# Optimization experiments

Hardware: AMD Instinct MI355X
Metric: run time of the kernel (lower is better)

The kernel has to match this reference:

```python
import math
import jax, jax.numpy as jnp
import numpy as np

N_HEADS = 8
FACTOR = 1


def setup_inputs() -> dict:
    key = jax.random.key(0)
    ks = jax.random.split(key, 8)
    B, L, D = 8, 2048, 512
    scale = 0.05
    return {
        "queries": jax.random.normal(ks[0], (B, L, D), jnp.float32),
        "keys": jax.random.normal(ks[1], (B, L, D), jnp.float32),
        "values": jax.random.normal(ks[2], (B, L, D), jnp.float32),
        "Wq": jax.random.normal(ks[3], (D, D), jnp.float32) * scale,
        "bq": jnp.zeros((D,), jnp.float32),
        "Wk": jax.random.normal(ks[4], (D, D), jnp.float32) * scale,
        "bk": jnp.zeros((D,), jnp.float32),
        "Wv": jax.random.normal(ks[5], (D, D), jnp.float32) * scale,
        "bv": jnp.zeros((D,), jnp.float32),
        "Wo": jax.random.normal(ks[6], (D, D), jnp.float32) * scale,
        "bo": jnp.zeros((D,), jnp.float32),
    }


def _autocorrelation(q, k, v):
    # q,k,v: [B, L, H, E]; L == S assumed (as built in setup_inputs)
    B, L, H, E = q.shape
    qp = jnp.transpose(q, (0, 2, 3, 1))  # [B,H,E,L]
    kp = jnp.transpose(k, (0, 2, 3, 1))
    vp = jnp.transpose(v, (0, 2, 3, 1))
    q_fft = jnp.fft.rfft(qp, axis=-1)
    k_fft = jnp.fft.rfft(kp, axis=-1)
    corr = jnp.fft.irfft(q_fft * jnp.conj(k_fft), n=L, axis=-1)  # [B,H,E,L]

    # training-path time-delay aggregation
    top_k = int(FACTOR * math.log(L))  # static python int
    mean_value = corr.mean(axis=(1, 2))  # [B, L]
    _, index = jax.lax.top_k(mean_value.mean(axis=0), top_k)  # [K] global delays
    weights = mean_value[:, index]  # [B, K]
    tmp_corr = jax.nn.softmax(weights, axis=-1)  # [B, K]
    # roll(v, -d) along last axis == gather at (t + d) mod L
    idx = (jnp.arange(L)[None, :] + index[:, None]) % L  # [K, L]
    patterns = vp[..., idx]  # [B,H,E,K,L]
    delays_agg = jnp.einsum('bhekl,bk->bhel', patterns, tmp_corr)  # [B,H,E,L]
    return jnp.transpose(delays_agg, (0, 3, 1, 2))  # [B,L,H,E]


def reference(queries, keys, values, Wq, bq, Wk, bk, Wv, bv, Wo, bo):
    B, L, Dm = queries.shape
    H = N_HEADS
    q = (queries @ Wq + bq).reshape(B, L, H, -1)
    k = (keys @ Wk + bk).reshape(B, L, H, -1)
    v = (values @ Wv + bv).reshape(B, L, H, -1)
    out = _autocorrelation(q, k, v).reshape(B, L, -1)
    return out @ Wo + bo
```

## Files before the change

kernel.cpp:

```cpp
#include <hip/hip_runtime.h>
#include <stdint.h>

#define BATCH 8
#define L_SEQ 2048
#define D_MODEL 512
#define TOPK 7
#define BM 128
#define BN 128
#define BK 32
#define LK 40
#define LT 136

typedef _Float16 f16x8 __attribute__((ext_vector_type(8)));
typedef __attribute__((ext_vector_type(4))) float f32x4;
typedef unsigned short u16;
typedef unsigned int u32;

__device__ __forceinline__ u16 f2h(float f) {
    union { _Float16 h; u16 u; } v; v.h = (_Float16)f; return v.u;
}
__device__ __forceinline__ float h2f(u16 b) {
    union { u16 u; _Float16 h; } v; v.u = b; return (float)v.h;
}

__device__ __forceinline__ void load_lds16(const u16* g, u16* l) {
    __builtin_amdgcn_global_load_lds(
        (const __attribute__((address_space(1))) u32*)(g),
        (__attribute__((address_space(3))) u32*)(l), 16, 0, 0);
}

__global__ __launch_bounds__(256) void gemm_qkv(
    const float* __restrict__ Xq, const float* __restrict__ Xk, const float* __restrict__ Xv,
    const u16* __restrict__ Wqt, const u16* __restrict__ Wkt, const u16* __restrict__ Wvt,
    const float* __restrict__ bq, const float* __restrict__ bk, const float* __restrict__ bv,
    u16* __restrict__ QT, u16* __restrict__ KT, u16* __restrict__ Vout)
{
    __shared__ __align__(16) u16 lA[BM * LK];
    __shared__ __align__(16) u16 lB[BN * LK];
    __shared__ __align__(16) u16 lT[64 * LT];

    const int tid = threadIdx.x;
    const int bn = blockIdx.x, bm = blockIdx.y, z = blockIdx.z;
    const int lane = tid & 63, wave = tid >> 6;
    const int wm = wave >> 1, wn = wave & 1;
    const int l15 = lane & 15, quad = lane >> 4;

    const float* A  = (z == 0) ? Xq  : (z == 1) ? Xk  : Xv;
    const u16*   Bt = (z == 0) ? Wqt : (z == 1) ? Wkt : Wvt;
    const float* bias = (z == 0) ? bq : (z == 1) ? bk : bv;

    f32x4 acc[4][4] = {};
    const int K = D_MODEL, N = D_MODEL;

    for (int k0 = 0; k0 < K; k0 += BK) {
        #pragma unroll
        for (int j = 0; j < 4; ++j) {
            int idx = tid + j * 256;
            int row = idx >> 3, c4 = (idx & 7) * 4;
            float4 va = *(const float4*)(A + (long)(bm * BM + row) * K + k0 + c4);
            ushort4 pa;
            pa.x = f2h(va.x); pa.y = f2h(va.y); pa.z = f2h(va.z); pa.w = f2h(va.w);
            *(ushort4*)&lA[row * LK + c4] = pa;
        }
        #pragma unroll
        for (int j = 0; j < 2; ++j) {
            int idx = tid + j * 256;
            int row = idx >> 2, c8 = (idx & 3) * 8;
            *(uint4*)&lB[row * LK + c8] =
                *(const uint4*)(Bt + (long)(bn * BN + row) * K + k0 + c8);
        }
        __syncthreads();

        f16x8 fa[4], fb[4];
        #pragma unroll
        for (int i = 0; i < 4; ++i)
            fa[i] = *(const f16x8*)&lA[(wm * 64 + i * 16 + l15) * LK + quad * 8];
        #pragma unroll
        for (int j = 0; j < 4; ++j)
            fb[j] = *(const f16x8*)&lB[(wn * 64 + j * 16 + l15) * LK + quad * 8];
        #pragma unroll
        for (int i = 0; i < 4; ++i)
            #pragma unroll
            for (int j = 0; j < 4; ++j)
                acc[i][j] = __builtin_amdgcn_mfma_f32_16x16x32_f16(fa[i], fb[j], acc[i][j], 0, 0, 0);
        __syncthreads();
    }

    if (z < 2) {
        u16* out = (z == 0) ? QT : KT;
        const int t0 = (bm * BM) & (L_SEQ - 1);
        const int bb = (bm * BM) >> 11;
        #pragma unroll
        for (int h = 0; h < 2; ++h) {
            __syncthreads();
            if (wn == h) {
                #pragma unroll
                for (int j = 0; j < 4; ++j) {
                    int dloc = j * 16 + l15;
                    float bvv = bias[bn * BN + h * 64 + dloc];
                    #pragma unroll
                    for (int i = 0; i < 4; ++i) {
                        int trow = wm * 64 + i * 16 + quad * 4;
                        #pragma unroll
                        for (int r = 0; r < 4; ++r)
                            lT[dloc * LT + trow + r] = f2h(acc[i][j][r] + bvv);
                    }
                }
            }
            __syncthreads();
            int dloc = tid >> 2, q4 = tid & 3;
            long base = ((long)(bb * D_MODEL + bn * BN + h * 64 + dloc)) * L_SEQ + t0;
            #pragma unroll
            for (int s = 0; s < 4; ++s) {
                int c = q4 * 4 + s;
                *(uint4*)(out + base + c * 8) = *(const uint4*)&lT[dloc * LT + c * 8];
            }
        }
    } else {
        #pragma unroll
        for (int i = 0; i < 4; ++i) {
            int row = bm * BM + wm * 64 + i * 16 + quad * 4;
            #pragma unroll
            for (int j = 0; j < 4; ++j) {
                int col = bn * BN + wn * 64 + j * 16 + l15;
                float bvv = bias[col];
                #pragma unroll
                for (int r = 0; r < 4; ++r)
                    Vout[(long)(row + r) * N + col] = f2h(acc[i][j][r] + bvv);
            }
        }
    }
}

__global__ __launch_bounds__(256, 4) void gemm_f16_out32(
    const u16* __restrict__ A, const u16* __restrict__ Bt,
    const float* __restrict__ bias, float* __restrict__ Cp, int N, int K)
{
    __shared__ __align__(16) u16 lA[BM * BK];
    __shared__ __align__(16) u16 lB[BN * BK];

    const int tid = threadIdx.x;
    const int bn = blockIdx.x, bm = blockIdx.y;
    const int lane = tid & 63, wave = tid >> 6;
    const int wm = wave >> 1, wn = wave & 1;
    const int l15 = lane & 15, quad = lane >> 4;

    const int s0 = wave * 64 + lane, s1 = s0 + 256;
    const int r0 = s0 >> 2, c0 = (s0 & 3) ^ ((r0 >> 1) & 3);
    const int r1 = s1 >> 2, c1 = (s1 & 3) ^ ((r1 >> 1) & 3);
    const u16* gA0 = A + (long)(bm * BM + r0) * K + c0 * 8;
    const u16* gA1 = A + (long)(bm * BM + r1) * K + c1 * 8;
    const u16* gB0 = Bt + (long)(bn * BN + r0) * K + c0 * 8;
    const u16* gB1 = Bt + (long)(bn * BN + r1) * K + c1 * 8;
    u16* lA0 = &lA[wave * 512]; u16* lA1 = &lA[2048 + wave * 512];
    u16* lB0 = &lB[wave * 512]; u16* lB1 = &lB[2048 + wave * 512];

    f32x4 acc[4][4] = {};

    for (int k0 = 0; k0 < K; k0 += BK) {
        load_lds16(gA0, lA0); load_lds16(gA1, lA1);
        load_lds16(gB0, lB0); load_lds16(gB1, lB1);
        gA0 += BK; gA1 += BK; gB0 += BK; gB1 += BK;
        __syncthreads();

        f16x8 fa[4], fb[4];
        #pragma unroll
        for (int i = 0; i < 4; ++i) {
            int m = wm * 64 + i * 16 + l15;
            int cs = quad ^ ((m >> 1) & 3);
            fa[i] = *(const f16x8*)&lA[m * 32 + cs * 8];
        }
        #pragma unroll
        for (int j = 0; j < 4; ++j) {
            int n = wn * 64 + j * 16 + l15;
            int cs = quad ^ ((n >> 1) & 3);
            fb[j] = *(const f16x8*)&lB[n * 32 + cs * 8];
        }
        #pragma unroll
        for (int i = 0; i < 4; ++i)
            #pragma unroll
            for (int j = 0; j < 4; ++j)
                acc[i][j] = __builtin_amdgcn_mfma_f32_16x16x32_f16(fa[i], fb[j], acc[i][j], 0, 0, 0);
        __syncthreads();
    }

    #pragma unroll
    for (int i = 0; i < 4; ++i) {
        int row = bm * BM + wm * 64 + i * 16 + quad * 4;
        #pragma unroll
        for (int j = 0; j < 4; ++j) {
            int col = bn * BN + wn * 64 + j * 16 + l15;
            float bvv = bias[col];
            #pragma unroll
            for (int r = 0; r < 4; ++r)
                Cp[(long)(row + r) * N + col] = acc[i][j][r] + bvv;
        }
    }
}

__global__ __launch_bounds__(256) void fft_corr_fwd(
    const u16* __restrict__ QT, const u16* __restrict__ KT, float* __restrict__ S)
{
    __shared__ float Zr[2048], Zi[2048];
    __shared__ float Sr[2048], Si[2048];
    __shared__ float Twr[1024], Twi[1024];
    const int tid = threadIdx.x;
    const int b = blockIdx.x >> 6, dg = blockIdx.x & 63;

    #pragma unroll
    for (int j = 0; j < 4; ++j) {
        int i = tid + j * 256;
        float ang = -6.28318530717958647692f * (float)i * (1.0f / 2048.0f);
        float sn, cs; __sincosf(ang, &sn, &cs);
        Twr[i] = cs; Twi[i] = sn;
    }
    #pragma unroll
    for (int j = 0; j < 8; ++j) { Sr[tid + j * 256] = 0.f; Si[tid + j * 256] = 0.f; }

    for (int g = 0; g < 8; ++g) {
        int d = dg * 8 + g;
        const u16* qrow = QT + ((long)b * D_MODEL + d) * L_SEQ;
        const u16* krow = KT + ((long)b * D_MODEL + d) * L_SEQ;
        __syncthreads();
        union { uint4 u; _Float16 h[8]; } xq, xk;
        xq.u = *(const uint4*)(qrow + tid * 8);
        xk.u = *(const uint4*)(krow + tid * 8);
        #pragma unroll
        for (int j = 0; j < 8; ++j) {
            int t = tid * 8 + j;
            int tr = (int)(__brev((unsigned)t) >> 21);
            Zr[tr] = (float)xq.h[j];
            Zi[tr] = (float)xk.h[j];
        }
        __syncthreads();
        for (int s = 0; s < 11; ++s) {
            #pragma unroll
            for (int j = 0; j < 4; ++j) {
                int idx = tid + j * 256;
                int pos = idx & ((1 << s) - 1);
                int i0 = ((idx >> s) << (s + 1)) + pos;
                int i1 = i0 + (1 << s);
                float wr = Twr[pos << (10 - s)], wi = Twi[pos << (10 - s)];
                float ar = Zr[i0], ai = Zi[i0];
                float br = Zr[i1], bi = Zi[i1];
                float tr_ = br * wr - bi * wi;
                float ti_ = br * wi + bi * wr;
                Zr[i0] = ar + tr_; Zi[i0] = ai + ti_;
                Zr[i1] = ar - tr_; Zi[i1] = ai - ti_;
            }
            __syncthreads();
        }
        #pragma unroll
        for (int j = 0; j < 8; ++j) {
            int f = tid + j * 256;
            int fm = (2048 - f) & 2047;
            float Xr = Zr[f], Xi = Zi[f], Xmr = Zr[fm], Xmi = Zi[fm];
            float qr = 0.5f * (Xr + Xmr), qi = 0.5f * (Xi - Xmi);
            float dr = Xr - Xmr,          di = Xi + Xmi;
            float kr = 0.5f * di,         ki = -0.5f * dr;
            Sr[f] += qr * kr + qi * ki;
            Si[f] += qi * kr - qr * ki;
        }
    }
    __syncthreads();
    #pragma unroll
    for (int j = 0; j < 8; ++j) {
        int f = tid + j * 256;
        atomicAdd(&S[((long)b * 2048 + f) * 2 + 0], Sr[f]);
        atomicAdd(&S[((long)b * 2048 + f) * 2 + 1], Si[f]);
    }
}

__global__ __launch_bounds__(256) void fft_corr_inv(
    const float* __restrict__ S, float* __restrict__ raw)
{
    __shared__ float Zr[2048], Zi[2048];
    __shared__ float Twr[1024], Twi[1024];
    const int tid = threadIdx.x;
    const int b = blockIdx.x;

    #pragma unroll
    for (int j = 0; j < 4; ++j) {
        int i = tid + j * 256;
        float ang = 6.28318530717958647692f * (float)i * (1.0f / 2048.0f);
        float sn, cs; __sincosf(ang, &sn, &cs);
        Twr[i] = cs; Twi[i] = sn;
    }
    #pragma unroll
    for (int j = 0; j < 8; ++j) {
        int f = tid + j * 256;
        int fr = (int)(__brev((unsigned)f) >> 21);
        Zr[fr] = S[((long)b * 2048 + f) * 2 + 0];
        Zi[fr] = S[((long)b * 2048 + f) * 2 + 1];
    }
    __syncthreads();
    for (int s = 0; s < 11; ++s) {
        #pragma unroll
        for (int j = 0; j < 4; ++j) {
            int idx = tid + j * 256;
            int pos = idx & ((1 << s) - 1);
            int i0 = ((idx >> s) << (s + 1)) + pos;
            int i1 = i0 + (1 << s);
            float wr = Twr[pos << (10 - s)], wi = Twi[pos << (10 - s)];
            float ar = Zr[i0], ai = Zi[i0];
            float br = Zr[i1], bi = Zi[i1];
            float tr_ = br * wr - bi * wi;
            float ti_ = br * wi + bi * wr;
            Zr[i0] = ar + tr_; Zi[i0] = ai + ti_;
            Zr[i1] = ar - tr_; Zi[i1] = ai - ti_;
        }
        __syncthreads();
    }
    #pragma unroll
    for (int j = 0; j < 8; ++j) {
        int t = tid + j * 256;
        raw[(long)b * 2048 + t] = Zr[t] * (1.0f / 2048.0f);
    }
}

__global__ __launch_bounds__(256) void transposeW(const float* __restrict__ src, u16* __restrict__ dst)
{
    __shared__ float t[32][33];
    int tx = threadIdx.x & 31, ty = threadIdx.x >> 5;
    int c0 = blockIdx.x * 32, r0 = blockIdx.y * 32;
    #pragma unroll
    for (int r = ty; r < 32; r += 8)
        t[r][tx] = src[(long)(r0 + r) * D_MODEL + c0 + tx];
    __syncthreads();
    #pragma unroll
    for (int r = ty; r < 32; r += 8)
        dst[(long)(c0 + r) * D_MODEL + r0 + tx] = f2h(t[tx][r]);
}

__global__ __launch_bounds__(256) void select_topk(
    const float* __restrict__ raw, int* __restrict__ selIdx, float* __restrict__ selW)
{
    __shared__ float g[L_SEQ];
    __shared__ float rv[256];
    __shared__ int   ri[256];
    __shared__ int   sidx[TOPK];
    __shared__ float wbuf[BATCH][TOPK];
    int tid = threadIdx.x;
    for (int t = tid; t < L_SEQ; t += 256) {
        float s = 0.0f;
        #pragma unroll
        for (int b = 0; b < BATCH; ++b) s += raw[b * L_SEQ + t];
        g[t] = s;
    }
    __syncthreads();
    for (int it = 0; it < TOPK; ++it) {
        float best = -1e30f; int bi = 0x7fffffff;
        for (int t = tid; t < L_SEQ; t += 256) {
            float v = g[t];
            if (v > best || (v == best && t < bi)) { best = v; bi = t; }
        }
        rv[tid] = best; ri[tid] = bi;
        __syncthreads();
        for (int s = 128; s > 0; s >>= 1) {
            if (tid < s) {
                float v2 = rv[tid + s]; int i2 = ri[tid + s];
                if (v2 > rv[tid] || (v2 == rv[tid] && i2 < ri[tid])) { rv[tid] = v2; ri[tid] = i2; }
            }
            __syncthreads();
        }
        if (tid == 0) { sidx[it] = ri[0]; g[ri[0]] = -1e30f; }
        __syncthreads();
    }
    if (tid < BATCH * TOPK) {
        int b = tid / TOPK, k = tid % TOPK;
        wbuf[b][k] = raw[b * L_SEQ + sidx[k]] * (1.0f / 512.0f);
    }
    __syncthreads();
    if (tid < BATCH) {
        float mx = -1e30f;
        #pragma unroll
        for (int k = 0; k < TOPK; ++k) mx = fmaxf(mx, wbuf[tid][k]);
        float e[TOPK]; float sum = 0.0f;
        #pragma unroll
        for (int k = 0; k < TOPK; ++k) { e[k] = expf(wbuf[tid][k] - mx); sum += e[k]; }
        #pragma unroll
        for (int k = 0; k < TOPK; ++k) selW[tid * TOPK + k] = e[k] / sum;
    }
    if (tid < TOPK) selIdx[tid] = sidx[tid];
}

__global__ __launch_bounds__(256) void gather_agg(
    const u16* __restrict__ V, const int* __restrict__ selIdx,
    const float* __restrict__ selW, u16* __restrict__ outB)
{
    __shared__ int si[TOPK];
    __shared__ float sw[TOPK];
    long flat = (long)blockIdx.x * 256 + threadIdx.x;
    int b  = (int)(flat >> 17);
    int l  = (int)((flat >> 6) & (L_SEQ - 1));
    int d8 = (int)(flat & 63);
    if (threadIdx.x < TOPK) {
        si[threadIdx.x] = selIdx[threadIdx.x];
        sw[threadIdx.x] = selW[b * TOPK + threadIdx.x];
    }
    __syncthreads();
    const uint4* v8 = (const uint4*)(V + (long)b * L_SEQ * D_MODEL);
    float a[8] = {0,0,0,0,0,0,0,0};
    #pragma unroll
    for (int k = 0; k < TOPK; ++k) {
        int src = (l + si[k]) & (L_SEQ - 1);
        union { uint4 u; _Float16 h[8]; } x;
        x.u = v8[src * 64 + d8];
        float w = sw[k];
        #pragma unroll
        for (int q = 0; q < 8; ++q) a[q] += w * (float)x.h[q];
    }
    union { uint4 u; _Float16 h[8]; } o;
    #pragma unroll
    for (int q = 0; q < 8; ++q) o.h[q] = (_Float16)a[q];
    ((uint4*)outB)[flat] = o.u;
}

extern "C" void kernel_launch(void* const* d_in, const int* in_sizes, int n_in,
                              void* d_out, int out_size, void* d_ws, size_t ws_size,
                              hipStream_t stream)
{
    (void)in_sizes; (void)n_in; (void)out_size; (void)ws_size;
    const float* Xq = (const float*)d_in[0];
    const float* Xk = (const float*)d_in[1];
    const float* Xv = (const float*)d_in[2];
    const float* Wq = (const float*)d_in[3];
    const float* bq = (const float*)d_in[4];
    const float* Wk = (const float*)d_in[5];
    const float* bk = (const float*)d_in[6];
    const float* Wv = (const float*)d_in[7];
    const float* bv = (const float*)d_in[8];
    const float* Wo = (const float*)d_in[9];
    const float* bo = (const float*)d_in[10];

    char* ws = (char*)d_ws;
    const long SLABH = (long)BATCH * L_SEQ * D_MODEL * sizeof(u16);
    u16* QT   = (u16*)(ws);
    u16* KT   = (u16*)(ws + SLABH);
    u16* Vf   = (u16*)(ws + 2 * SLABH);
    u16* attn = (u16*)(ws + 3 * SLABH);
    const long WSZ = (long)D_MODEL * D_MODEL;
    u16* Wt   = (u16*)(ws + 4 * SLABH);
    u16* Wqt = Wt + 0 * WSZ; u16* Wkt = Wt + 1 * WSZ;
    u16* Wvt = Wt + 2 * WSZ; u16* Wot = Wt + 3 * WSZ;
    float* S   = (float*)(ws + 4 * SLABH + 4 * WSZ * sizeof(u16));
    float* raw = S + (long)BATCH * L_SEQ * 2;
    int*   sIdx = (int*)(raw + (long)BATCH * L_SEQ);
    float* sW   = (float*)(sIdx + 8);

    dim3 tb(256);
    transposeW<<<dim3(16, 16), tb, 0, stream>>>(Wq, Wqt);
    transposeW<<<dim3(16, 16), tb, 0, stream>>>(Wk, Wkt);
    transposeW<<<dim3(16, 16), tb, 0, stream>>>(Wv, Wvt);
    transposeW<<<dim3(16, 16), tb, 0, stream>>>(Wo, Wot);
    hipMemsetAsync(S, 0, (long)BATCH * L_SEQ * 2 * sizeof(float), stream);

    dim3 gP(D_MODEL / BN, (BATCH * L_SEQ) / BM, 3);
    gemm_qkv<<<gP, tb, 0, stream>>>(Xq, Xk, Xv, Wqt, Wkt, Wvt, bq, bk, bv, QT, KT, Vf);

    fft_corr_fwd<<<dim3(512), tb, 0, stream>>>(QT, KT, S);
    fft_corr_inv<<<dim3(BATCH), tb, 0, stream>>>(S, raw);

    select_topk<<<1, tb, 0, stream>>>(raw, sIdx, sW);

    gather_agg<<<(BATCH * L_SEQ * D_MODEL / 8) / 256, tb, 0, stream>>>(Vf, sIdx, sW, attn);

    dim3 gO(D_MODEL / BN, (BATCH * L_SEQ) / BM, 1);
    gemm_f16_out32<<<gO, tb, 0, stream>>>(attn, Wot, bo, (float*)d_out, D_MODEL, D_MODEL);
}
```

Baseline: 357.9 us.

## Prefetch QKV GEMM tiles, radix-4 FFT, fuse inverse FFT with top-k, merge transposes

The QKV GEMM now loads the next K-tile into registers while the current tile is computed, aliases its LDS buffers, and remaps blocks to a 1D grid grouped for L2 locality. The FFT switches from radix-2 to radix-4 stages, halving the barrier count. The per-batch inverse FFT and the top-k kernel are merged into one finalize kernel. It runs a single inverse FFT on the batch-summed spectrum and computes the per-batch weights at the selected delays by direct DFT sums. The four weight-transpose launches become one. This cuts launches and synchronisations, but the finalize kernel is a single block doing serial DFT work.

```diff
diff --git a/kernel.cpp b/kernel.cpp
--- a/kernel.cpp
+++ b/kernel.cpp
@@ -19,9 +19,6 @@
 __device__ __forceinline__ u16 f2h(float f) {
     union { _Float16 h; u16 u; } v; v.h = (_Float16)f; return v.u;
 }
-__device__ __forceinline__ float h2f(u16 b) {
-    union { u16 u; _Float16 h; } v; v.u = b; return (float)v.h;
-}
 
 __device__ __forceinline__ void load_lds16(const u16* g, u16* l) {
     __builtin_amdgcn_global_load_lds(
@@ -35,12 +32,18 @@
     const float* __restrict__ bq, const float* __restrict__ bk, const float* __restrict__ bv,
     u16* __restrict__ QT, u16* __restrict__ KT, u16* __restrict__ Vout)
 {
-    __shared__ __align__(16) u16 lA[BM * LK];
-    __shared__ __align__(16) u16 lB[BN * LK];
-    __shared__ __align__(16) u16 lT[64 * LT];
+    __shared__ __align__(16) char smem[20480];
+    u16* lA = (u16*)smem;
+    u16* lB = (u16*)(smem + 10240);
+    u16* lT = (u16*)smem;
 
     const int tid = threadIdx.x;
-    const int bn = blockIdx.x, bm = blockIdx.y, z = blockIdx.z;
+    const int id = blockIdx.x;
+    const int bmL = id & 7;
+    const int bn  = (id >> 3) & 3;
+    const int bmH = (id >> 5) & 15;
+    const int z   = id >> 9;
+    const int bm  = bmH * 8 + bmL;
     const int lane = tid & 63, wave = tid >> 6;
     const int wm = wave >> 1, wn = wave & 1;
     const int l15 = lane & 15, quad = lane >> 4;
@@ -49,27 +52,48 @@
     const u16*   Bt = (z == 0) ? Wqt : (z == 1) ? Wkt : Wvt;
     const float* bias = (z == 0) ? bq : (z == 1) ? bk : bv;
 
+    float4 pA[4]; uint4 pB[2];
+    #pragma unroll
+    for (int j = 0; j < 4; ++j) {
+        int idx = tid + j * 256; int row = idx >> 3, c4 = (idx & 7) * 4;
+        pA[j] = *(const float4*)(A + (long)(bm * BM + row) * D_MODEL + c4);
+    }
+    #pragma unroll
+    for (int j = 0; j < 2; ++j) {
+        int idx = tid + j * 256; int row = idx >> 2, c8 = (idx & 3) * 8;
+        pB[j] = *(const uint4*)(Bt + (long)(bn * BN + row) * D_MODEL + c8);
+    }
+
     f32x4 acc[4][4] = {};
-    const int K = D_MODEL, N = D_MODEL;
-
-    for (int k0 = 0; k0 < K; k0 += BK) {
+
+    for (int k0 = 0; k0 < D_MODEL; k0 += BK) {
         #pragma unroll
         for (int j = 0; j < 4; ++j) {
-            int idx = tid + j * 256;
-            int row = idx >> 3, c4 = (idx & 7) * 4;
-            float4 va = *(const float4*)(A + (long)(bm * BM + row) * K + k0 + c4);
+            int idx = tid + j * 256; int row = idx >> 3, c4 = (idx & 7) * 4;
             ushort4 pa;
-            pa.x = f2h(va.x); pa.y = f2h(va.y); pa.z = f2h(va.z); pa.w = f2h(va.w);
+            pa.x = f2h(pA[j].x); pa.y = f2h(pA[j].y);
+            pa.z = f2h(pA[j].z); pa.w = f2h(pA[j].w);
             *(ushort4*)&lA[row * LK + c4] = pa;
         }
         #pragma unroll
         for (int j = 0; j < 2; ++j) {
-            int idx = tid + j * 256;
-            int row = idx >> 2, c8 = (idx & 3) * 8;
-            *(uint4*)&lB[row * LK + c8] =
-                *(const uint4*)(Bt + (long)(bn * BN + row) * K + k0 + c8);
-        }
-        __syncthreads();
+            int idx = tid + j * 256; int row = idx >> 2, c8 = (idx & 3) * 8;
+            *(uint4*)&lB[row * LK + c8] = pB[j];
+        }
+        __syncthreads();
+
+        if (k0 + BK < D_MODEL) {
+            #pragma unroll
+            for (int j = 0; j < 4; ++j) {
+                int idx = tid + j * 256; int row = idx >> 3, c4 = (idx & 7) * 4;
+                pA[j] = *(const float4*)(A + (long)(bm * BM + row) * D_MODEL + k0 + BK + c4);
+            }
+            #pragma unroll
+            for (int j = 0; j < 2; ++j) {
+                int idx = tid + j * 256; int row = idx >> 2, c8 = (idx & 3) * 8;
+                pB[j] = *(const uint4*)(Bt + (long)(bn * BN + row) * D_MODEL + k0 + BK + c8);
+            }
+        }
 
         f16x8 fa[4], fb[4];
         #pragma unroll
@@ -126,7 +150,7 @@
                 float bvv = bias[col];
                 #pragma unroll
                 for (int r = 0; r < 4; ++r)
-                    Vout[(long)(row + r) * N + col] = f2h(acc[i][j][r] + bvv);
+                    Vout[(long)(row + r) * D_MODEL + col] = f2h(acc[i][j][r] + bvv);
             }
         }
     }
@@ -198,6 +222,51 @@
     }
 }
 
+__device__ __forceinline__ void fft2048_lds(
+    float* Zr, float* Zi, const float* Twr, const float* Twi, int tid)
+{
+    #pragma unroll
+    for (int s = 0; s < 10; s += 2) {
+        #pragma unroll
+        for (int u = 0; u < 2; ++u) {
+            int idx = tid + u * 256;
+            int d1 = 1 << s;
+            int pos = idx & (d1 - 1);
+            int i0 = ((idx >> s) << (s + 2)) + pos;
+            float w1r = Twr[pos << (10 - s)], w1i = Twi[pos << (10 - s)];
+            float w2r = Twr[pos << (9 - s)],  w2i = Twi[pos << (9 - s)];
+            int p2 = pos + d1;
+            float w3r = Twr[p2 << (9 - s)],   w3i = Twi[p2 << (9 - s)];
+            float ar = Zr[i0],          ai = Zi[i0];
+            float br = Zr[i0 + d1],     bi = Zi[i0 + d1];
+            float cr = Zr[i0 + 2 * d1], ci = Zi[i0 + 2 * d1];
+            float dr = Zr[i0 + 3 * d1], di = Zi[i0 + 3 * d1];
+            float t1r = br * w1r - bi * w1i, t1i = br * w1i + bi * w1r;
+            float Ar = ar + t1r, Ai = ai + t1i, Br = ar - t1r, Bi = ai - t1i;
+            float t2r = dr * w1r - di * w1i, t2i = dr * w1i + di * w1r;
+            float Cr = cr + t2r, Ci = ci + t2i, Dr = cr - t2r, Di = ci - t2i;
+            float u1r = Cr * w2r - Ci * w2i, u1i = Cr * w2i + Ci * w2r;
+            float u2r = Dr * w3r - Di * w3i, u2i = Dr * w3i + Di * w3r;
+            Zr[i0]          = Ar + u1r; Zi[i0]          = Ai + u1i;
+            Zr[i0 + 2 * d1] = Ar - u1r; Zi[i0 + 2 * d1] = Ai - u1i;
+            Zr[i0 + d1]     = Br + u2r; Zi[i0 + d1]     = Bi + u2i;
+            Zr[i0 + 3 * d1] = Br - u2r; Zi[i0 + 3 * d1] = Bi - u2i;
+        }
+        __syncthreads();
+    }
+    #pragma unroll
+    for (int j = 0; j < 4; ++j) {
+        int idx = tid + j * 256;
+        float wr = Twr[idx], wi = Twi[idx];
+        float ar = Zr[idx], ai = Zi[idx];
+        float br = Zr[idx + 1024], bi = Zi[idx + 1024];
+        float tr = br * wr - bi * wi, ti = br * wi + bi * wr;
+        Zr[idx] = ar + tr; Zi[idx] = ai + ti;
+        Zr[idx + 1024] = ar - tr; Zi[idx + 1024] = ai - ti;
+    }
+    __syncthreads();
+}
+
 __global__ __launch_bounds__(256) void fft_corr_fwd(
     const u16* __restrict__ QT, const u16* __restrict__ KT, float* __restrict__ S)
 {
@@ -233,23 +302,7 @@
             Zi[tr] = (float)xk.h[j];
         }
         __syncthreads();
-        for (int s = 0; s < 11; ++s) {
-            #pragma unroll
-            for (int j = 0; j < 4; ++j) {
-                int idx = tid + j * 256;
-                int pos = idx & ((1 << s) - 1);
-                int i0 = ((idx >> s) << (s + 1)) + pos;
-                int i1 = i0 + (1 << s);
-                float wr = Twr[pos << (10 - s)], wi = Twi[pos << (10 - s)];
-                float ar = Zr[i0], ai = Zi[i0];
-                float br = Zr[i1], bi = Zi[i1];
-                float tr_ = br * wr - bi * wi;
-                float ti_ = br * wi + bi * wr;
-                Zr[i0] = ar + tr_; Zi[i0] = ai + ti_;
-                Zr[i1] = ar - tr_; Zi[i1] = ai - ti_;
-            }
-            __syncthreads();
-        }
+        fft2048_lds(Zr, Zi, Twr, Twi, tid);
         #pragma unroll
         for (int j = 0; j < 8; ++j) {
             int f = tid + j * 256;
@@ -271,13 +324,17 @@
     }
 }
 
-__global__ __launch_bounds__(256) void fft_corr_inv(
-    const float* __restrict__ S, float* __restrict__ raw)
+__global__ __launch_bounds__(256) void finalize(
+    const float* __restrict__ S, int* __restrict__ selIdx, float* __restrict__ selW)
 {
     __shared__ float Zr[2048], Zi[2048];
     __shared__ float Twr[1024], Twi[1024];
+    __shared__ float rv[256];
+    __shared__ int   ri[256];
+    __shared__ int   sidx[TOPK];
+    __shared__ float pbuf[256];
+    __shared__ float wbuf[BATCH][TOPK];
     const int tid = threadIdx.x;
-    const int b = blockIdx.x;
 
     #pragma unroll
     for (int j = 0; j < 4; ++j) {
@@ -289,69 +346,21 @@
     #pragma unroll
     for (int j = 0; j < 8; ++j) {
         int f = tid + j * 256;
+        float sr = 0.f, si = 0.f;
+        #pragma unroll
+        for (int b = 0; b < BATCH; ++b) {
+            sr += S[((long)b * 2048 + f) * 2 + 0];
+            si += S[((long)b * 2048 + f) * 2 + 1];
+        }
         int fr = (int)(__brev((unsigned)f) >> 21);
-        Zr[fr] = S[((long)b * 2048 + f) * 2 + 0];
-        Zi[fr] = S[((long)b * 2048 + f) * 2 + 1];
-    }
-    __syncthreads();
-    for (int s = 0; s < 11; ++s) {
-        #pragma unroll
-        for (int j = 0; j < 4; ++j) {
-            int idx = tid + j * 256;
-            int pos = idx & ((1 << s) - 1);
-            int i0 = ((idx >> s) << (s + 1)) + pos;
-            int i1 = i0 + (1 << s);
-            float wr = Twr[pos << (10 - s)], wi = Twi[pos << (10 - s)];
-            float ar = Zr[i0], ai = Zi[i0];
-            float br = Zr[i1], bi = Zi[i1];
-            float tr_ = br * wr - bi * wi;
-            float ti_ = br * wi + bi * wr;
-            Zr[i0] = ar + tr_; Zi[i0] = ai + ti_;
-            Zr[i1] = ar - tr_; Zi[i1] = ai - ti_;
-        }
-        __syncthreads();
-    }
-    #pragma unroll
-    for (int j = 0; j < 8; ++j) {
-        int t = tid + j * 256;
-        raw[(long)b * 2048 + t] = Zr[t] * (1.0f / 2048.0f);
-    }
-}
-
-__global__ __launch_bounds__(256) void transposeW(const float* __restrict__ src, u16* __restrict__ dst)
-{
-    __shared__ float t[32][33];
-    int tx = threadIdx.x & 31, ty = threadIdx.x >> 5;
-    int c0 = blockIdx.x * 32, r0 = blockIdx.y * 32;
-    #pragma unroll
-    for (int r = ty; r < 32; r += 8)
-        t[r][tx] = src[(long)(r0 + r) * D_MODEL + c0 + tx];
-    __syncthreads();
-    #pragma unroll
-    for (int r = ty; r < 32; r += 8)
-        dst[(long)(c0 + r) * D_MODEL + r0 + tx] = f2h(t[tx][r]);
-}
-
-__global__ __launch_bounds__(256) void select_topk(
-    const float* __restrict__ raw, int* __restrict__ selIdx, float* __restrict__ selW)
-{
-    __shared__ float g[L_SEQ];
-    __shared__ float rv[256];
-    __shared__ int   ri[256];
-    __shared__ int   sidx[TOPK];
-    __shared__ float wbuf[BATCH][TOPK];
-    int tid = threadIdx.x;
-    for (int t = tid; t < L_SEQ; t += 256) {
-        float s = 0.0f;
-        #pragma unroll
-        for (int b = 0; b < BATCH; ++b) s += raw[b * L_SEQ + t];
-        g[t] = s;
-    }
-    __syncthreads();
+        Zr[fr] = sr; Zi[fr] = si;
+    }
+    __syncthreads();
+    fft2048_lds(Zr, Zi, Twr, Twi, tid);
     for (int it = 0; it < TOPK; ++it) {
         float best = -1e30f; int bi = 0x7fffffff;
         for (int t = tid; t < L_SEQ; t += 256) {
-            float v = g[t];
+            float v = Zr[t];
             if (v > best || (v == best && t < bi)) { best = v; bi = t; }
         }
         rv[tid] = best; ri[tid] = bi;
@@ -363,25 +372,60 @@
             }
             __syncthreads();
         }
-        if (tid == 0) { sidx[it] = ri[0]; g[ri[0]] = -1e30f; }
-        __syncthreads();
-    }
+        if (tid == 0) { sidx[it] = ri[0]; Zr[ri[0]] = -1e30f; }
+        __syncthreads();
+    }
+    int pair = tid >> 2, i4 = tid & 3;
+    float part = 0.f;
+    if (pair < BATCH * TOPK) {
+        int b = pair / TOPK, k = pair % TOPK, tau = sidx[k];
+        for (int n = 0; n < 512; ++n) {
+            int f = i4 + 4 * n;
+            int m = (f * tau) & 2047;
+            float cr, ci;
+            if (m < 1024) { cr = Twr[m]; ci = Twi[m]; }
+            else          { cr = -Twr[m - 1024]; ci = -Twi[m - 1024]; }
+            part += S[((long)b * 2048 + f) * 2 + 0] * cr
+                  - S[((long)b * 2048 + f) * 2 + 1] * ci;
+        }
+    }
+    pbuf[tid] = part;
+    __syncthreads();
     if (tid < BATCH * TOPK) {
-        int b = tid / TOPK, k = tid % TOPK;
-        wbuf[b][k] = raw[b * L_SEQ + sidx[k]] * (1.0f / 512.0f);
+        float s = pbuf[tid * 4] + pbuf[tid * 4 + 1] + pbuf[tid * 4 + 2] + pbuf[tid * 4 + 3];
+        wbuf[tid / TOPK][tid % TOPK] = s * (1.0f / (2048.0f * 512.0f));
     }
     __syncthreads();
     if (tid < BATCH) {
         float mx = -1e30f;
         #pragma unroll
         for (int k = 0; k < TOPK; ++k) mx = fmaxf(mx, wbuf[tid][k]);
-        float e[TOPK]; float sum = 0.0f;
+        float e[TOPK]; float sum = 0.f;
         #pragma unroll
         for (int k = 0; k < TOPK; ++k) { e[k] = expf(wbuf[tid][k] - mx); sum += e[k]; }
         #pragma unroll
         for (int k = 0; k < TOPK; ++k) selW[tid * TOPK + k] = e[k] / sum;
     }
     if (tid < TOPK) selIdx[tid] = sidx[tid];
+}
+
+__global__ __launch_bounds__(256) void transposeW4(
+    const float* __restrict__ Wq, const float* __restrict__ Wk,
+    const float* __restrict__ Wv, const float* __restrict__ Wo, u16* __restrict__ dstBase)
+{
+    __shared__ float t[32][33];
+    const int z = blockIdx.z;
+    const float* src = (z == 0) ? Wq : (z == 1) ? Wk : (z == 2) ? Wv : Wo;
+    u16* dst = dstBase + (long)z * D_MODEL * D_MODEL;
+    int tx = threadIdx.x & 31, ty = threadIdx.x >> 5;
+    int c0 = blockIdx.x * 32, r0 = blockIdx.y * 32;
+    #pragma unroll
+    for (int r = ty; r < 32; r += 8)
+        t[r][tx] = src[(long)(r0 + r) * D_MODEL + c0 + tx];
+    __syncthreads();
+    #pragma unroll
+    for (int r = ty; r < 32; r += 8)
+        dst[(long)(c0 + r) * D_MODEL + r0 + tx] = f2h(t[tx][r]);
 }
 
 __global__ __launch_bounds__(256) void gather_agg(
@@ -444,24 +488,17 @@
     u16* Wqt = Wt + 0 * WSZ; u16* Wkt = Wt + 1 * WSZ;
     u16* Wvt = Wt + 2 * WSZ; u16* Wot = Wt + 3 * WSZ;
     float* S   = (float*)(ws + 4 * SLABH + 4 * WSZ * sizeof(u16));
-    float* raw = S + (long)BATCH * L_SEQ * 2;
-    int*   sIdx = (int*)(raw + (long)BATCH * L_SEQ);
+    int*   sIdx = (int*)(S + (long)BATCH * L_SEQ * 2);
     float* sW   = (float*)(sIdx + 8);
 
     dim3 tb(256);
-    transposeW<<<dim3(16, 16), tb, 0, stream>>>(Wq, Wqt);
-    transposeW<<<dim3(16, 16), tb, 0, stream>>>(Wk, Wkt);
-    transposeW<<<dim3(16, 16), tb, 0, stream>>>(Wv, Wvt);
-    transposeW<<<dim3(16, 16), tb, 0, stream>>>(Wo, Wot);
+    transposeW4<<<dim3(16, 16, 4), tb, 0, stream>>>(Wq, Wk, Wv, Wo, Wt);
     hipMemsetAsync(S, 0, (long)BATCH * L_SEQ * 2 * sizeof(float), stream);
 
-    dim3 gP(D_MODEL / BN, (BATCH * L_SEQ) / BM, 3);
-    gemm_qkv<<<gP, tb, 0, stream>>>(Xq, Xk, Xv, Wqt, Wkt, Wvt, bq, bk, bv, QT, KT, Vf);
+    gemm_qkv<<<dim3(1536), tb, 0, stream>>>(Xq, Xk, Xv, Wqt, Wkt, Wvt, bq, bk, bv, QT, KT, Vf);
 
     fft_corr_fwd<<<dim3(512), tb, 0, stream>>>(QT, KT, S);
-    fft_corr_inv<<<dim3(BATCH), tb, 0, stream>>>(S, raw);
-
-    select_topk<<<1, tb, 0, stream>>>(raw, sIdx, sW);
+    finalize<<<dim3(1), tb, 0, stream>>>(S, sIdx, sW);
 
     gather_agg<<<(BATCH * L_SEQ * D_MODEL / 8) / 256, tb, 0, stream>>>(Vf, sIdx, sW, attn);
 
```

After: 408.7 us. 14.2% more time.

## Fuse delay aggregation into output GEMM, radix-4 FFT stages, merge weight transposes

Applied to the files above, without the earlier changes.

Removes the separate gather_agg kernel and its attn intermediate by computing the weighted top-k delay sum directly while staging the A tile of the output projection GEMM. Replaces the radix-2 FFT loop with paired radix-4 stages to halve the number of LDS passes and barriers, and merges the four weight transposes into one launch. The fused GEMM recomputes the gather for each of the four N-tile blocks, which multiplies V reads, and it drops the async global_load_lds path for A.

```diff
diff --git a/kernel.cpp b/kernel.cpp
--- a/kernel.cpp
+++ b/kernel.cpp
@@ -19,9 +19,6 @@
 __device__ __forceinline__ u16 f2h(float f) {
     union { _Float16 h; u16 u; } v; v.h = (_Float16)f; return v.u;
 }
-__device__ __forceinline__ float h2f(u16 b) {
-    union { u16 u; _Float16 h; } v; v.u = b; return (float)v.h;
-}
 
 __device__ __forceinline__ void load_lds16(const u16* g, u16* l) {
     __builtin_amdgcn_global_load_lds(
@@ -50,14 +47,13 @@
     const float* bias = (z == 0) ? bq : (z == 1) ? bk : bv;
 
     f32x4 acc[4][4] = {};
-    const int K = D_MODEL, N = D_MODEL;
-
-    for (int k0 = 0; k0 < K; k0 += BK) {
+
+    for (int k0 = 0; k0 < D_MODEL; k0 += BK) {
         #pragma unroll
         for (int j = 0; j < 4; ++j) {
             int idx = tid + j * 256;
             int row = idx >> 3, c4 = (idx & 7) * 4;
-            float4 va = *(const float4*)(A + (long)(bm * BM + row) * K + k0 + c4);
+            float4 va = *(const float4*)(A + (long)(bm * BM + row) * D_MODEL + k0 + c4);
             ushort4 pa;
             pa.x = f2h(va.x); pa.y = f2h(va.y); pa.z = f2h(va.z); pa.w = f2h(va.w);
             *(ushort4*)&lA[row * LK + c4] = pa;
@@ -67,7 +63,7 @@
             int idx = tid + j * 256;
             int row = idx >> 2, c8 = (idx & 3) * 8;
             *(uint4*)&lB[row * LK + c8] =
-                *(const uint4*)(Bt + (long)(bn * BN + row) * K + k0 + c8);
+                *(const uint4*)(Bt + (long)(bn * BN + row) * D_MODEL + k0 + c8);
         }
         __syncthreads();
 
@@ -126,18 +122,21 @@
                 float bvv = bias[col];
                 #pragma unroll
                 for (int r = 0; r < 4; ++r)
-                    Vout[(long)(row + r) * N + col] = f2h(acc[i][j][r] + bvv);
+                    Vout[(long)(row + r) * D_MODEL + col] = f2h(acc[i][j][r] + bvv);
             }
         }
     }
 }
 
-__global__ __launch_bounds__(256, 4) void gemm_f16_out32(
-    const u16* __restrict__ A, const u16* __restrict__ Bt,
-    const float* __restrict__ bias, float* __restrict__ Cp, int N, int K)
-{
-    __shared__ __align__(16) u16 lA[BM * BK];
+__global__ __launch_bounds__(256) void gemm_out_fused(
+    const u16* __restrict__ V, const u16* __restrict__ Bt,
+    const int* __restrict__ selIdx, const float* __restrict__ selW,
+    const float* __restrict__ bias, float* __restrict__ Cp)
+{
+    __shared__ __align__(16) u16 lA[BM * LK];
     __shared__ __align__(16) u16 lB[BN * BK];
+    __shared__ int   si[TOPK];
+    __shared__ float sw[BATCH][TOPK];
 
     const int tid = threadIdx.x;
     const int bn = blockIdx.x, bm = blockIdx.y;
@@ -145,31 +144,50 @@
     const int wm = wave >> 1, wn = wave & 1;
     const int l15 = lane & 15, quad = lane >> 4;
 
+    if (tid < TOPK) si[tid] = selIdx[tid];
+    if (tid < BATCH * TOPK) sw[tid / TOPK][tid % TOPK] = selW[tid];
+
     const int s0 = wave * 64 + lane, s1 = s0 + 256;
     const int r0 = s0 >> 2, c0 = (s0 & 3) ^ ((r0 >> 1) & 3);
     const int r1 = s1 >> 2, c1 = (s1 & 3) ^ ((r1 >> 1) & 3);
-    const u16* gA0 = A + (long)(bm * BM + r0) * K + c0 * 8;
-    const u16* gA1 = A + (long)(bm * BM + r1) * K + c1 * 8;
-    const u16* gB0 = Bt + (long)(bn * BN + r0) * K + c0 * 8;
-    const u16* gB1 = Bt + (long)(bn * BN + r1) * K + c1 * 8;
-    u16* lA0 = &lA[wave * 512]; u16* lA1 = &lA[2048 + wave * 512];
+    const u16* gB0 = Bt + (long)(bn * BN + r0) * D_MODEL + c0 * 8;
+    const u16* gB1 = Bt + (long)(bn * BN + r1) * D_MODEL + c1 * 8;
     u16* lB0 = &lB[wave * 512]; u16* lB1 = &lB[2048 + wave * 512];
 
+    __syncthreads();
+
     f32x4 acc[4][4] = {};
 
-    for (int k0 = 0; k0 < K; k0 += BK) {
-        load_lds16(gA0, lA0); load_lds16(gA1, lA1);
+    for (int k0 = 0; k0 < D_MODEL; k0 += BK) {
         load_lds16(gB0, lB0); load_lds16(gB1, lB1);
-        gA0 += BK; gA1 += BK; gB0 += BK; gB1 += BK;
+        gB0 += BK; gB1 += BK;
+        #pragma unroll
+        for (int j = 0; j < 2; ++j) {
+            int idx = tid + j * 256;
+            int row = idx >> 2, c8 = (idx & 3) * 8;
+            int gr = bm * BM + row;
+            int b = gr >> 11, l = gr & (L_SEQ - 1);
+            float a[8] = {0,0,0,0,0,0,0,0};
+            #pragma unroll
+            for (int k = 0; k < TOPK; ++k) {
+                int src = (l + si[k]) & (L_SEQ - 1);
+                union { uint4 u; _Float16 h[8]; } x;
+                x.u = *(const uint4*)(V + ((long)b * L_SEQ + src) * D_MODEL + k0 + c8);
+                float w = sw[b][k];
+                #pragma unroll
+                for (int q = 0; q < 8; ++q) a[q] += w * (float)x.h[q];
+            }
+            union { uint4 u; u16 s[8]; } o;
+            #pragma unroll
+            for (int q = 0; q < 8; ++q) o.s[q] = f2h(a[q]);
+            *(uint4*)&lA[row * LK + c8] = o.u;
+        }
         __syncthreads();
 
         f16x8 fa[4], fb[4];
         #pragma unroll
-        for (int i = 0; i < 4; ++i) {
-            int m = wm * 64 + i * 16 + l15;
-            int cs = quad ^ ((m >> 1) & 3);
-            fa[i] = *(const f16x8*)&lA[m * 32 + cs * 8];
-        }
+        for (int i = 0; i < 4; ++i)
+            fa[i] = *(const f16x8*)&lA[(wm * 64 + i * 16 + l15) * LK + quad * 8];
         #pragma unroll
         for (int j = 0; j < 4; ++j) {
             int n = wn * 64 + j * 16 + l15;
@@ -193,9 +211,54 @@
             float bvv = bias[col];
             #pragma unroll
             for (int r = 0; r < 4; ++r)
-                Cp[(long)(row + r) * N + col] = acc[i][j][r] + bvv;
-        }
-    }
+                Cp[(long)(row + r) * D_MODEL + col] = acc[i][j][r] + bvv;
+        }
+    }
+}
+
+__device__ __forceinline__ void fft2048_lds(
+    float* Zr, float* Zi, const float* Twr, const float* Twi, int tid)
+{
+    #pragma unroll
+    for (int s = 0; s < 10; s += 2) {
+        #pragma unroll
+        for (int u = 0; u < 2; ++u) {
+            int idx = tid + u * 256;
+            int d1 = 1 << s;
+            int pos = idx & (d1 - 1);
+            int i0 = ((idx >> s) << (s + 2)) + pos;
+            float w1r = Twr[pos << (10 - s)], w1i = Twi[pos << (10 - s)];
+            float w2r = Twr[pos << (9 - s)],  w2i = Twi[pos << (9 - s)];
+            int p2 = pos + d1;
+            float w3r = Twr[p2 << (9 - s)],   w3i = Twi[p2 << (9 - s)];
+            float ar = Zr[i0],          ai = Zi[i0];
+            float br = Zr[i0 + d1],     bi = Zi[i0 + d1];
+            float cr = Zr[i0 + 2 * d1], ci = Zi[i0 + 2 * d1];
+            float dr = Zr[i0 + 3 * d1], di = Zi[i0 + 3 * d1];
+            float t1r = br * w1r - bi * w1i, t1i = br * w1i + bi * w1r;
+            float Ar = ar + t1r, Ai = ai + t1i, Br = ar - t1r, Bi = ai - t1i;
+            float t2r = dr * w1r - di * w1i, t2i = dr * w1i + di * w1r;
+            float Cr = cr + t2r, Ci = ci + t2i, Dr = cr - t2r, Di = ci - t2i;
+            float u1r = Cr * w2r - Ci * w2i, u1i = Cr * w2i + Ci * w2r;
+            float u2r = Dr * w3r - Di * w3i, u2i = Dr * w3i + Di * w3r;
+            Zr[i0]          = Ar + u1r; Zi[i0]          = Ai + u1i;
+            Zr[i0 + 2 * d1] = Ar - u1r; Zi[i0 + 2 * d1] = Ai - u1i;
+            Zr[i0 + d1]     = Br + u2r; Zi[i0 + d1]     = Bi + u2i;
+            Zr[i0 + 3 * d1] = Br - u2r; Zi[i0 + 3 * d1] = Bi - u2i;
+        }
+        __syncthreads();
+    }
+    #pragma unroll
+    for (int j = 0; j < 4; ++j) {
+        int idx = tid + j * 256;
+        float wr = Twr[idx], wi = Twi[idx];
+        float ar = Zr[idx], ai = Zi[idx];
+        float br = Zr[idx + 1024], bi = Zi[idx + 1024];
+        float tr = br * wr - bi * wi, ti = br * wi + bi * wr;
+        Zr[idx] = ar + tr; Zi[idx] = ai + ti;
+        Zr[idx + 1024] = ar - tr; Zi[idx + 1024] = ai - ti;
+    }
+    __syncthreads();
 }
 
 __global__ __launch_bounds__(256) void fft_corr_fwd(
@@ -233,23 +296,7 @@
             Zi[tr] = (float)xk.h[j];
         }
         __syncthreads();
-        for (int s = 0; s < 11; ++s) {
-            #pragma unroll
-            for (int j = 0; j < 4; ++j) {
-                int idx = tid + j * 256;
-                int pos = idx & ((1 << s) - 1);
-                int i0 = ((idx >> s) << (s + 1)) + pos;
-                int i1 = i0 + (1 << s);
-                float wr = Twr[pos << (10 - s)], wi = Twi[pos << (10 - s)];
-                float ar = Zr[i0], ai = Zi[i0];
-                float br = Zr[i1], bi = Zi[i1];
-                float tr_ = br * wr - bi * wi;
-                float ti_ = br * wi + bi * wr;
-                Zr[i0] = ar + tr_; Zi[i0] = ai + ti_;
-                Zr[i1] = ar - tr_; Zi[i1] = ai - ti_;
-            }
-            __syncthreads();
-        }
+        fft2048_lds(Zr, Zi, Twr, Twi, tid);
         #pragma unroll
         for (int j = 0; j < 8; ++j) {
             int f = tid + j * 256;
@@ -294,23 +341,7 @@
         Zi[fr] = S[((long)b * 2048 + f) * 2 + 1];
     }
     __syncthreads();
-    for (int s = 0; s < 11; ++s) {
-        #pragma unroll
-        for (int j = 0; j < 4; ++j) {
-            int idx = tid + j * 256;
-            int pos = idx & ((1 << s) - 1);
-            int i0 = ((idx >> s) << (s + 1)) + pos;
-            int i1 = i0 + (1 << s);
-            float wr = Twr[pos << (10 - s)], wi = Twi[pos << (10 - s)];
-            float ar = Zr[i0], ai = Zi[i0];
-            float br = Zr[i1], bi = Zi[i1];
-            float tr_ = br * wr - bi * wi;
-            float ti_ = br * wi + bi * wr;
-            Zr[i0] = ar + tr_; Zi[i0] = ai + ti_;
-            Zr[i1] = ar - tr_; Zi[i1] = ai - ti_;
-        }
-        __syncthreads();
-    }
+    fft2048_lds(Zr, Zi, Twr, Twi, tid);
     #pragma unroll
     for (int j = 0; j < 8; ++j) {
         int t = tid + j * 256;
@@ -318,9 +349,14 @@
     }
 }
 
-__global__ __launch_bounds__(256) void transposeW(const float* __restrict__ src, u16* __restrict__ dst)
+__global__ __launch_bounds__(256) void transposeW4(
+    const float* __restrict__ Wq, const float* __restrict__ Wk,
+    const float* __restrict__ Wv, const float* __restrict__ Wo, u16* __restrict__ dstBase)
 {
     __shared__ float t[32][33];
+    const int z = blockIdx.z;
+    const float* src = (z == 0) ? Wq : (z == 1) ? Wk : (z == 2) ? Wv : Wo;
+    u16* dst = dstBase + (long)z * D_MODEL * D_MODEL;
     int tx = threadIdx.x & 31, ty = threadIdx.x >> 5;
     int c0 = blockIdx.x * 32, r0 = blockIdx.y * 32;
     #pragma unroll
@@ -382,38 +418,6 @@
         for (int k = 0; k < TOPK; ++k) selW[tid * TOPK + k] = e[k] / sum;
     }
     if (tid < TOPK) selIdx[tid] = sidx[tid];
-}
-
-__global__ __launch_bounds__(256) void gather_agg(
-    const u16* __restrict__ V, const int* __restrict__ selIdx,
-    const float* __restrict__ selW, u16* __restrict__ outB)
-{
-    __shared__ int si[TOPK];
-    __shared__ float sw[TOPK];
-    long flat = (long)blockIdx.x * 256 + threadIdx.x;
-    int b  = (int)(flat >> 17);
-    int l  = (int)((flat >> 6) & (L_SEQ - 1));
-    int d8 = (int)(flat & 63);
-    if (threadIdx.x < TOPK) {
-        si[threadIdx.x] = selIdx[threadIdx.x];
-        sw[threadIdx.x] = selW[b * TOPK + threadIdx.x];
-    }
-    __syncthreads();
-    const uint4* v8 = (const uint4*)(V + (long)b * L_SEQ * D_MODEL);
-    float a[8] = {0,0,0,0,0,0,0,0};
-    #pragma unroll
-    for (int k = 0; k < TOPK; ++k) {
-        int src = (l + si[k]) & (L_SEQ - 1);
-        union { uint4 u; _Float16 h[8]; } x;
-        x.u = v8[src * 64 + d8];
-        float w = sw[k];
-        #pragma unroll
-        for (int q = 0; q < 8; ++q) a[q] += w * (float)x.h[q];
-    }
-    union { uint4 u; _Float16 h[8]; } o;
-    #pragma unroll
-    for (int q = 0; q < 8; ++q) o.h[q] = (_Float16)a[q];
-    ((uint4*)outB)[flat] = o.u;
 }
 
 extern "C" void kernel_launch(void* const* d_in, const int* in_sizes, int n_in,
@@ -438,21 +442,17 @@
     u16* QT   = (u16*)(ws);
     u16* KT   = (u16*)(ws + SLABH);
     u16* Vf   = (u16*)(ws + 2 * SLABH);
-    u16* attn = (u16*)(ws + 3 * SLABH);
     const long WSZ = (long)D_MODEL * D_MODEL;
-    u16* Wt   = (u16*)(ws + 4 * SLABH);
+    u16* Wt   = (u16*)(ws + 3 * SLABH);
     u16* Wqt = Wt + 0 * WSZ; u16* Wkt = Wt + 1 * WSZ;
     u16* Wvt = Wt + 2 * WSZ; u16* Wot = Wt + 3 * WSZ;
-    float* S   = (float*)(ws + 4 * SLABH + 4 * WSZ * sizeof(u16));
+    float* S   = (float*)(ws + 3 * SLABH + 4 * WSZ * sizeof(u16));
     float* raw = S + (long)BATCH * L_SEQ * 2;
     int*   sIdx = (int*)(raw + (long)BATCH * L_SEQ);
     float* sW   = (float*)(sIdx + 8);
 
     dim3 tb(256);
-    transposeW<<<dim3(16, 16), tb, 0, stream>>>(Wq, Wqt);
-    transposeW<<<dim3(16, 16), tb, 0, stream>>>(Wk, Wkt);
-    transposeW<<<dim3(16, 16), tb, 0, stream>>>(Wv, Wvt);
-    transposeW<<<dim3(16, 16), tb, 0, stream>>>(Wo, Wot);
+    transposeW4<<<dim3(16, 16, 4), tb, 0, stream>>>(Wq, Wk, Wv, Wo, Wt);
     hipMemsetAsync(S, 0, (long)BATCH * L_SEQ * 2 * sizeof(float), stream);
 
     dim3 gP(D_MODEL / BN, (BATCH * L_SEQ) / BM, 3);
@@ -460,11 +460,8 @@
 
     fft_corr_fwd<<<dim3(512), tb, 0, stream>>>(QT, KT, S);
     fft_corr_inv<<<dim3(BATCH), tb, 0, stream>>>(S, raw);
-
     select_topk<<<1, tb, 0, stream>>>(raw, sIdx, sW);
 
-    gather_agg<<<(BATCH * L_SEQ * D_MODEL / 8) / 256, tb, 0, stream>>>(Vf, sIdx, sW, attn);
-
     dim3 gO(D_MODEL / BN, (BATCH * L_SEQ) / BM, 1);
-    gemm_f16_out32<<<gO, tb, 0, stream>>>(attn, Wot, bo, (float*)d_out, D_MODEL, D_MODEL);
-}
+    gemm_out_fused<<<gO, tb, 0, stream>>>(Vf, Wot, sIdx, sW, bo, (float*)d_out);
+}
```

Measured after the change: 344.8 us. -3.6%, faster.
